# Performance work log

Measured on AMD Instinct MI355X. Metric: run time of the kernel, lower is better.

## Reference

```python
import jax, jax.numpy as jnp
import numpy as np

B, L, T = 64, 256, 800
NMEL, PRE, ARNN, DRNN, ENC, ATT, NF, K = 80, 256, 512, 512, 512, 128, 32, 31
ZP = 0.1  # zoneout prob (eval-mode expected-value interpolation)


def setup_inputs() -> dict:
    key = jax.random.key(0)
    ks = iter(jax.random.split(key, 32))
    def p(shape, s=0.05):
        return jax.random.normal(next(ks), shape, dtype=jnp.float32) * s
    inp = {
        'encoder_out': jax.random.normal(next(ks), (B, L, ENC), dtype=jnp.float32),
        'lengths': jax.random.randint(next(ks), (B,), L // 2, L + 1),
        'mels': jax.random.normal(next(ks), (B, T, NMEL), dtype=jnp.float32),
        # prenet: 3 bias-free linears with relu (eval: dropout off)
        'Wp1': p((PRE, NMEL)), 'Wp2': p((PRE, PRE)), 'Wp3': p((PRE, PRE)),
        # attention LSTMCell: input = prenet_dim + enc = 768
        'aWih': p((4 * ARNN, PRE + ENC)), 'aWhh': p((4 * ARNN, ARNN)),
        'abih': jnp.zeros((4 * ARNN,)), 'abhh': jnp.zeros((4 * ARNN,)),
        # decoder LSTMCell: input = att_rnn + enc = 1024
        'dWih': p((4 * DRNN, ARNN + ENC)), 'dWhh': p((4 * DRNN, DRNN)),
        'dbih': jnp.zeros((4 * DRNN,)), 'dbhh': jnp.zeros((4 * DRNN,)),
        # location-sensitive attention (all bias-free)
        'Wq': p((ATT, ARNN)), 'Wm': p((ATT, ENC)),
        'Wconv': p((NF, 2, K)), 'Wloc': p((ATT, NF)), 'v': p((1, ATT)),
        # output projection + gate
        'Wout': p((NMEL, DRNN + ENC)), 'bout': jnp.zeros((NMEL,)),
        'Wgate': p((1, DRNN + ENC)), 'bgate': jnp.zeros((1,)),
    }
    return inp


def _lstm(x, h, c, Wih, Whh, bih, bhh):
    g = x @ Wih.T + h @ Whh.T + (bih + bhh)
    i, f, gg, o = jnp.split(g, 4, axis=-1)
    c2 = jax.nn.sigmoid(f) * c + jax.nn.sigmoid(i) * jnp.tanh(gg)
    return jax.nn.sigmoid(o) * jnp.tanh(c2), c2


def _zoneout(new, old):
    return ZP * old + (1.0 - ZP) * new


def decoder_forward(encoder_out, lengths, mels, Wp1, Wp2, Wp3,
                    aWih, aWhh, abih, abhh, dWih, dWhh, dbih, dbhh,
                    Wq, Wm, Wconv, Wloc, v, Wout, bout, Wgate, bgate):
    b, l, _ = encoder_out.shape
    t = mels.shape[1]
    processed_memory = encoder_out @ Wm.T                       # (B,L,ATT)
    mask = jnp.arange(l)[None, :] >= lengths[:, None]           # True = padded
    # teacher forcing inputs: shift mels right by one zero frame
    dec_in = jnp.concatenate(
        [jnp.zeros((b, 1, NMEL), encoder_out.dtype), mels[:, :t - 1]], axis=1)
    xs = jnp.swapaxes(dec_in, 0, 1)                             # (T,B,NMEL)

    def step(carry, frame):
        ah, ac, dh, dc, ctx, aw, aws = carry
        x = jax.nn.relu(jax.nn.relu(jax.nn.relu(frame @ Wp1.T) @ Wp2.T) @ Wp3.T)
        ah2, ac2 = _lstm(jnp.concatenate([x, ctx], -1), ah, ac, aWih, aWhh, abih, abhh)
        ah2, ac2 = _zoneout(ah2, ah), _zoneout(ac2, ac)
        # location features: conv over (B,2,L)
        aw_cat = jnp.stack([aw, aws], axis=1)
        loc = jax.lax.conv_general_dilated(
            aw_cat, Wconv, window_strides=(1,), padding=[((K - 1) // 2,) * 2],
            dimension_numbers=('NCH', 'OIH', 'NCH'))                # (B,NF,L)
        ploc = jnp.swapaxes(loc, 1, 2) @ Wloc.T                      # (B,L,ATT)
        e = jnp.tanh(ah2[:, None, :] @ Wq.T + processed_memory + ploc)
        energies = jnp.squeeze(e @ v.T, -1)                          # (B,L)
        energies = jnp.where(mask, jnp.float32(-1e9), energies)
        w = jax.nn.softmax(energies, axis=-1)
        ctx2 = jnp.einsum('bl,ble->be', w, encoder_out)
        aws2 = aws + w
        dh2, dc2 = _lstm(jnp.concatenate([ah2, ctx2], -1), dh, dc, dWih, dWhh, dbih, dbhh)
        dh2, dc2 = _zoneout(dh2, dh), _zoneout(dc2, dc)
        dhc = jnp.concatenate([dh2, ctx2], axis=-1)
        mel = dhc @ Wout.T + bout
        gate = jnp.squeeze(dhc @ Wgate.T + bgate, -1)
        return (ah2, ac2, dh2, dc2, ctx2, w, aws2), (mel, gate, w)

    z = lambda *s: jnp.zeros(s, encoder_out.dtype)
    carry0 = (z(b, ARNN), z(b, ARNN), z(b, DRNN), z(b, DRNN), z(b, ENC), z(b, l), z(b, l))
    _, (mel_t, gate_t, align_t) = jax.lax.scan(step, carry0, xs)
    return (jnp.swapaxes(mel_t, 0, 1),      # (B,T,NMEL)
            jnp.swapaxes(gate_t, 0, 1),     # (B,T)
            jnp.swapaxes(align_t, 0, 1))    # (B,T,L)


def reference(encoder_out, lengths, mels, Wp1, Wp2, Wp3,
              aWih, aWhh, abih, abhh, dWih, dWhh, dbih, dbhh,
              Wq, Wm, Wconv, Wloc, v, Wout, bout, Wgate, bgate):
    return decoder_forward(encoder_out, lengths, mels, Wp1, Wp2, Wp3,
                           aWih, aWhh, abih, abhh, dWih, dWhh, dbih, dbhh,
                           Wq, Wm, Wconv, Wloc, v, Wout, bout, Wgate, bgate)
```

## Files before the change

kernel.cpp:

```cpp
#include <hip/hip_runtime.h>


#define DEV_INLINE __device__ __forceinline__

constexpr int TB = 800;

constexpr size_t PMT_O  = 0;
constexpr size_t WQT_O  = 2228224;
constexpr size_t LOCF_O = 2293760;
constexpr size_t Y1_O   = 2818048;
constexpr size_t Y2_O   = 2834432;
constexpr size_t XR_O   = 2850816;
constexpr size_t AH_O   = 2883584;
constexpr size_t AC_O   = 2949120;
constexpr size_t DH_O   = 3014656;
constexpr size_t DC_O   = 3080192;
constexpr size_t CTX_O  = 3145728;
constexpr size_t AW_O   = 3211264;
constexpr size_t AWS_O  = 3244032;
constexpr size_t BAR_O  = 3276800;
constexpr size_t ZERO_N = 991232;

constexpr size_t MEL_O  = 0;
constexpr size_t GATE_O = 4096000;
constexpr size_t ALG_O  = 4147200;

DEV_INLINE float sigf(float x)     { return 1.0f / (1.0f + __expf(-x)); }
DEV_INLINE float tanhfast(float x) { float e = __expf(2.0f * x); return 1.0f - 2.0f / (e + 1.0f); }

DEV_INLINE void stc(float* p, float v) {
  __hip_atomic_store(p, v, __ATOMIC_RELAXED, __HIP_MEMORY_SCOPE_AGENT);
}

struct Params {
  const float* enc; const int* len; const float* mels;
  const float* Wp1; const float* Wp2; const float* Wp3;
  const float* aWih; const float* aWhh; const float* abih; const float* abhh;
  const float* dWih; const float* dWhh; const float* dbih; const float* dbhh;
  const float* Wconv; const float* Wloc; const float* v;
  const float* Wout; const float* bout; const float* Wgate; const float* bgate;
  float* ws; float* out;
};

DEV_INLINE void gbar(unsigned* bar, int blk, bool iscap, unsigned e)
{
  __syncthreads();
  if (threadIdx.x == 0) {
    const unsigned g = (unsigned)blk >> 5;
    unsigned a = __hip_atomic_fetch_add(bar + g * 64, 1u, __ATOMIC_RELAXED, __HIP_MEMORY_SCOPE_AGENT);
    if (a == e * 32u - 1u)
      __hip_atomic_fetch_add(bar + 512, 1u, __ATOMIC_RELAXED, __HIP_MEMORY_SCOPE_AGENT);
    if (iscap) {
      while (__hip_atomic_load(bar + 512, __ATOMIC_RELAXED, __HIP_MEMORY_SCOPE_AGENT) < e * 8u)
        __builtin_amdgcn_s_sleep(1);
      __builtin_amdgcn_fence(__ATOMIC_ACQUIRE, "agent");
      const unsigned nc = __hip_atomic_load(bar + 2176, __ATOMIC_RELAXED, __HIP_MEMORY_SCOPE_AGENT);
      unsigned c = __hip_atomic_fetch_add(bar + 576, 1u, __ATOMIC_RELAXED, __HIP_MEMORY_SCOPE_AGENT);
      if (c == e * nc - 1u) {
#pragma unroll
        for (unsigned i = 0; i < 8; ++i)
          __hip_atomic_store(bar + 640 + i * 64, e, __ATOMIC_RELAXED, __HIP_MEMORY_SCOPE_AGENT);
      }
    }
    {
      const unsigned g2 = (unsigned)blk >> 5;
      while (__hip_atomic_load(bar + 640 + g2 * 64, __ATOMIC_RELAXED, __HIP_MEMORY_SCOPE_AGENT) < e)
        __builtin_amdgcn_s_sleep(4);
    }
  }
  __syncthreads();
  asm volatile("buffer_inv sc0\n\ts_waitcnt vmcnt(0)" ::: "memory");
}

DEV_INLINE void gseg16(float* __restrict__ acc,
                       const float* __restrict__ inT,
                       const float* __restrict__ W, const int ldw, const int wcol0,
                       const int u0, const int segk0, const int seglen,
                       const int ks, const int ke, const int lane)
{
  const int a0 = ks > segk0 ? ks : segk0;
  const int a1 = (ke < segk0 + seglen) ? ke : (segk0 + seglen);
  if (a0 >= a1) return;
  const float* __restrict__ ip = inT + (size_t)(a0 - segk0) * 64 + lane;
  const int n = a1 - a0;
  const float* wp[16];
#pragma unroll
  for (int j = 0; j < 16; ++j) {
    const int row = u0 + (j >> 2) + 512 * (j & 3);
    wp[j] = W + (size_t)row * ldw + (wcol0 + (a0 - segk0));
  }
  for (int k = 0; k < n; k += 4) {
    const float x0 = ip[(k + 0) * 64];
    const float x1 = ip[(k + 1) * 64];
    const float x2 = ip[(k + 2) * 64];
    const float x3 = ip[(k + 3) * 64];
#pragma unroll
    for (int j = 0; j < 16; ++j)
      acc[j] += x0 * wp[j][k] + x1 * wp[j][k + 1] + x2 * wp[j][k + 2] + x3 * wp[j][k + 3];
  }
}

template<int NO>
DEV_INLINE void gseg(float* __restrict__ acc,
                     const float* __restrict__ inT,
                     const float* __restrict__ W, const int ldw, const int wcol0,
                     const int* __restrict__ rows, const int segk0, const int seglen,
                     const int ks, const int ke, const int lane)
{
  const int a0 = ks > segk0 ? ks : segk0;
  const int a1 = (ke < segk0 + seglen) ? ke : (segk0 + seglen);
  if (a0 >= a1) return;
  const float* __restrict__ ip = inT + (size_t)(a0 - segk0) * 64 + lane;
  const int n = a1 - a0;
  const float* wp[NO];
#pragma unroll
  for (int j = 0; j < NO; ++j)
    wp[j] = W + (size_t)rows[j] * ldw + (wcol0 + (a0 - segk0));
  for (int k = 0; k < n; k += 4) {
    const float x0 = ip[(k + 0) * 64];
    const float x1 = ip[(k + 1) * 64];
    const float x2 = ip[(k + 2) * 64];
    const float x3 = ip[(k + 3) * 64];
#pragma unroll
    for (int j = 0; j < NO; ++j)
      acc[j] += x0 * wp[j][k] + x1 * wp[j][k + 1] + x2 * wp[j][k + 2] + x3 * wp[j][k + 3];
  }
}

__global__ __launch_bounds__(256) void init_kernel(const float* __restrict__ Wq,
                                                   float* __restrict__ ws)
{
  const int i = blockIdx.x * 256 + threadIdx.x;
  {
    const int k = i >> 7, a = i & 127;
    ws[WQT_O + i] = Wq[a * 512 + k];
  }
  for (size_t idx = i; idx < ZERO_N; idx += 65536)
    ws[LOCF_O + idx] = 0.0f;
}

__global__ __launch_bounds__(256) void prenet_kernel(const float* __restrict__ mels,
                                                     const float* __restrict__ Wp1,
                                                     const float* __restrict__ Wp2,
                                                     const float* __restrict__ Wp3,
                                                     float* __restrict__ xb)
{
  __shared__ float smem[16384];
  const int t = blockIdx.x;
  const int tid = threadIdx.x;
  const int lane = tid & 63;
  const int wv = __builtin_amdgcn_readfirstlane(tid >> 6);

  if (t == 0) {
    for (int i = tid; i < 5200; i += 256) smem[i] = 0.0f;
  } else {
    for (int i = tid; i < 5120; i += 256) {
      const int b = i / 80, k = i - b * 80;
      smem[k * 65 + b] = mels[((size_t)b * TB + (t - 1)) * 80 + k];
    }
  }
  __syncthreads();

  float va[8][8];
#pragma unroll
  for (int g = 0; g < 8; ++g) {
    const int u0 = wv * 64 + g * 8;
    float acc[8] = {};
    for (int k = 0; k < 80; ++k) {
      const float x = smem[k * 65 + lane];
#pragma unroll
      for (int j = 0; j < 8; ++j) acc[j] += x * Wp1[(u0 + j) * 80 + k];
    }
#pragma unroll
    for (int j = 0; j < 8; ++j) va[g][j] = fmaxf(acc[j], 0.0f);
  }
  __syncthreads();
#pragma unroll
  for (int g = 0; g < 8; ++g)
#pragma unroll
    for (int j = 0; j < 8; ++j) smem[(wv * 64 + g * 8 + j) * 64 + lane] = va[g][j];
  __syncthreads();

#pragma unroll
  for (int g = 0; g < 8; ++g) {
    const int u0 = wv * 64 + g * 8;
    float acc[8] = {};
    for (int k = 0; k < 256; ++k) {
      const float x = smem[k * 64 + lane];
#pragma unroll
      for (int j = 0; j < 8; ++j) acc[j] += x * Wp2[(u0 + j) * 256 + k];
    }
#pragma unroll
    for (int j = 0; j < 8; ++j) va[g][j] = fmaxf(acc[j], 0.0f);
  }
  __syncthreads();
#pragma unroll
  for (int g = 0; g < 8; ++g)
#pragma unroll
    for (int j = 0; j < 8; ++j) smem[(wv * 64 + g * 8 + j) * 64 + lane] = va[g][j];
  __syncthreads();

#pragma unroll
  for (int g = 0; g < 8; ++g) {
    const int u0 = wv * 64 + g * 8;
    float acc[8] = {};
    for (int k = 0; k < 256; ++k) {
      const float x = smem[k * 64 + lane];
#pragma unroll
      for (int j = 0; j < 8; ++j) acc[j] += x * Wp3[(u0 + j) * 256 + k];
    }
#pragma unroll
    for (int j = 0; j < 8; ++j)
      xb[((size_t)t * 256 + (u0 + j)) * 64 + lane] = fmaxf(acc[j], 0.0f);
  }
}

__global__ __launch_bounds__(256) void pm_kernel(const float* __restrict__ enc,
                                                 const float* __restrict__ Wm,
                                                 float* __restrict__ pmT)
{
  __shared__ float encL[64 * 129];
  const int b = blockIdx.x >> 2;
  const int l0 = (blockIdx.x & 3) * 64;
  const int tid = threadIdx.x;
  const int lane = tid & 63;
  const int wv = __builtin_amdgcn_readfirstlane(tid >> 6);

  float acc[4][8];
#pragma unroll
  for (int ai = 0; ai < 4; ++ai)
#pragma unroll
    for (int j = 0; j < 8; ++j) acc[ai][j] = 0.0f;

  for (int kc = 0; kc < 4; ++kc) {
    __syncthreads();
    for (int i = tid; i < 64 * 128; i += 256) {
      const int l = i >> 7, k = i & 127;
      encL[l * 129 + k] = enc[((size_t)b * 256 + l0 + l) * 512 + kc * 128 + k];
    }
    __syncthreads();
#pragma unroll
    for (int ai = 0; ai < 4; ++ai) {
      const int agrp = (ai * 4 + wv) * 8;
      for (int k = 0; k < 128; ++k) {
        const float x = encL[lane * 129 + k];
#pragma unroll
        for (int j = 0; j < 8; ++j)
          acc[ai][j] += x * Wm[(size_t)(agrp + j) * 512 + kc * 128 + k];
      }
    }
  }
#pragma unroll
  for (int ai = 0; ai < 4; ++ai) {
    const int agrp = (ai * 4 + wv) * 8;
#pragma unroll
    for (int j = 0; j < 8; ++j)
      pmT[((size_t)b * 128 + agrp + j) * 256 + l0 + lane] = acc[ai][j];
  }
}


DEV_INLINE void f_dgates4(int u0, int tid, int lane, int wv,
                          const float* __restrict__ ah, const float* __restrict__ dh,
                          float* __restrict__ gdL, const Params& p, float* sm)
{
  float acc[16] = {};
  const int ks = wv * 256, ke = ks + 256;
  gseg16(acc, ah, p.dWih, 1024, 0, u0, 0,   512, ks, ke, lane);
  gseg16(acc, dh, p.dWhh, 512,  0, u0, 512, 512, ks, ke, lane);
#pragma unroll
  for (int j = 0; j < 16; ++j) sm[(wv * 16 + j) * 64 + lane] = acc[j];
  __syncthreads();
  {
    const int m = tid & 63, uq = tid >> 6;
    const int u = u0 + uq;
#pragma unroll
    for (int q = 0; q < 4; ++q) {
      const int j = uq * 4 + q;
      gdL[j * 64 + m] = sm[j * 64 + m] + sm[(16 + j) * 64 + m] + sm[(32 + j) * 64 + m] + sm[(48 + j) * 64 + m]
                      + p.dbih[u + 512 * q] + p.dbhh[u + 512 * q];
    }
  }
  __syncthreads();
}

DEV_INLINE void f_dfin4(int u0, int tid, int lane, int wv,
                        const float* __restrict__ ctx, const float* __restrict__ gdL,
                        float* __restrict__ dh_o, float* __restrict__ dhL, float* __restrict__ dcL,
                        const Params& p, float* sm)
{
  float acc[16] = {};
  const int ks = wv * 128, ke = ks + 128;
  gseg16(acc, ctx, p.dWih, 1024, 512, u0, 0, 512, ks, ke, lane);
#pragma unroll
  for (int j = 0; j < 16; ++j) sm[(wv * 16 + j) * 64 + lane] = acc[j];
  __syncthreads();
  {
    const int m = tid & 63, uq = tid >> 6;
    const int u = u0 + uq;
    float g[4];
#pragma unroll
    for (int q = 0; q < 4; ++q) {
      const int j = uq * 4 + q;
      g[q] = sm[j * 64 + m] + sm[(16 + j) * 64 + m] + sm[(32 + j) * 64 + m] + sm[(48 + j) * 64 + m]
           + gdL[j * 64 + m];
    }
    const float ho = dhL[uq * 64 + m], co = dcL[uq * 64 + m];
    const float c2 = sigf(g[1]) * co + sigf(g[0]) * tanhfast(g[2]);
    const float h2 = sigf(g[3]) * tanhfast(c2);
    const float hn = 0.1f * ho + 0.9f * h2;
    const float cn = 0.1f * co + 0.9f * c2;
    stc(dh_o + (size_t)u * 64 + m, hn);
    dhL[uq * 64 + m] = hn;
    dcL[uq * 64 + m] = cn;
  }
  __syncthreads();
}

DEV_INLINE void f_alstm4(int u0, int tid, int lane, int wv,
                         const float* __restrict__ xt, const float* __restrict__ ctx,
                         const float* __restrict__ ahg,
                         float* __restrict__ ah_o, float* __restrict__ ahL, float* __restrict__ acL,
                         const Params& p, float* sm)
{
  float acc[16] = {};
  const int ks = wv * 320, ke = ks + 320;
  gseg16(acc, xt,  p.aWih, 768, 0,   u0, 0,   256, ks, ke, lane);
  gseg16(acc, ctx, p.aWih, 768, 256, u0, 256, 512, ks, ke, lane);
  gseg16(acc, ahg, p.aWhh, 512, 0,   u0, 768, 512, ks, ke, lane);
#pragma unroll
  for (int j = 0; j < 16; ++j) sm[(wv * 16 + j) * 64 + lane] = acc[j];
  __syncthreads();
  {
    const int m = tid & 63, uq = tid >> 6;
    const int u = u0 + uq;
    float g[4];
#pragma unroll
    for (int q = 0; q < 4; ++q) {
      const int j = uq * 4 + q;
      g[q] = sm[j * 64 + m] + sm[(16 + j) * 64 + m] + sm[(32 + j) * 64 + m] + sm[(48 + j) * 64 + m]
           + p.abih[u + 512 * q] + p.abhh[u + 512 * q];
    }
    const float ho = ahL[uq * 64 + m], co = acL[uq * 64 + m];
    const float c2 = sigf(g[1]) * co + sigf(g[0]) * tanhfast(g[2]);
    const float h2 = sigf(g[3]) * tanhfast(c2);
    const float hn = 0.1f * ho + 0.9f * h2;
    const float cn = 0.1f * co + 0.9f * c2;
    stc(ah_o + (size_t)u * 64 + m, hn);
    ahL[uq * 64 + m] = hn;
    acL[uq * 64 + m] = cn;
  }
  __syncthreads();
}

DEV_INLINE void f_mel(int c0, int tid, int lane, int wv, int tm1,
                      const float* __restrict__ dh, const float* __restrict__ ctx,
                      const Params& p, float* sm)
{
  int rows[4] = {c0, c0 + 1, c0 + 2, c0 + 3};
  float acc[4] = {};
  const int ks = wv * 256, ke = ks + 256;
  gseg<4>(acc, dh,  p.Wout, 1024, 0,   rows, 0,   512, ks, ke, lane);
  gseg<4>(acc, ctx, p.Wout, 1024, 512, rows, 512, 512, ks, ke, lane);
#pragma unroll
  for (int j = 0; j < 4; ++j) sm[(wv * 4 + j) * 64 + lane] = acc[j];
  __syncthreads();
  {
    const int m = tid & 63, c = tid >> 6;
    const float val = sm[c * 64 + m] + sm[(4 + c) * 64 + m] + sm[(8 + c) * 64 + m] + sm[(12 + c) * 64 + m]
                    + p.bout[c0 + c];
    stc(p.out + MEL_O + ((size_t)m * TB + tm1) * 80 + c0 + c, val);
  }
  __syncthreads();
}

DEV_INLINE void f_gate(int tid, int lane, int wv, int tm1,
                       const float* __restrict__ dh, const float* __restrict__ ctx,
                       const Params& p, float* sm)
{
  float acc[1] = {};
  int rows1[1] = {0};
  const int ks = wv * 256, ke = ks + 256;
  gseg<1>(acc, dh,  p.Wgate, 1024, 0,   rows1, 0,   512, ks, ke, lane);
  gseg<1>(acc, ctx, p.Wgate, 1024, 512, rows1, 512, 512, ks, ke, lane);
  sm[wv * 64 + lane] = acc[0];
  __syncthreads();
  if (tid < 64) {
    const float val = sm[tid] + sm[64 + tid] + sm[128 + tid] + sm[192 + tid] + p.bgate[0];
    stc(p.out + GATE_O + (size_t)tid * TB + tm1, val);
  }
  __syncthreads();
}

DEV_INLINE void f_conv(int b, int tid,
                       const float* __restrict__ aw, const float* __restrict__ aws,
                       float* __restrict__ locF, const Params& p, float* sm)
{
  float* awL  = sm;
  float* awsL = sm + 290;
  if (tid < 15) { awL[tid] = 0.0f; awsL[tid] = 0.0f; awL[271 + tid] = 0.0f; awsL[271 + tid] = 0.0f; }
  awL[15 + tid]  = aw[b * 256 + tid];
  awsL[15 + tid] = aws[b * 256 + tid];
  __syncthreads();
  float awv[31], awsv[31];
#pragma unroll
  for (int k = 0; k < 31; ++k) { awv[k] = awL[tid + k]; awsv[k] = awsL[tid + k]; }
  float* dst = locF + ((size_t)b * 256 + tid) * 32;
  for (int f = 0; f < 32; ++f) {
    const float* wc = p.Wconv + f * 62;
    float lf = 0.0f;
#pragma unroll
    for (int k = 0; k < 31; ++k) lf += awv[k] * wc[k] + awsv[k] * wc[31 + k];
    stc(dst + f, lf);
  }
  __syncthreads();
}

DEV_INLINE void f_energy(int b, int t, int tid, int lane, int wv,
                         const float* __restrict__ ah, const float* __restrict__ aws_p,
                         float* __restrict__ ctx_o, float* __restrict__ aw_o,
                         float* __restrict__ aws_o,
                         const float* __restrict__ pmT, const float* __restrict__ wqT,
                         const float* __restrict__ locF, const Params& p, float* sm)
{
  float* ahL = sm;
  float* qpL = sm + 512;
  float* qL  = sm + 768;
  float* red = sm + 896;
  float* wL  = sm + 912;
  ahL[tid]       = ah[(size_t)tid * 64 + b];
  ahL[tid + 256] = ah[(size_t)(tid + 256) * 64 + b];
  __syncthreads();
  {
    const int a = tid & 127, h = tid >> 7;
    float qp = 0.0f;
    const float* wq = wqT + (size_t)(h * 256) * 128 + a;
    const float* xv = ahL + h * 256;
    for (int k = 0; k < 256; k += 4)
      qp += wq[(k + 0) * 128] * xv[k + 0] + wq[(k + 1) * 128] * xv[k + 1]
          + wq[(k + 2) * 128] * xv[k + 2] + wq[(k + 3) * 128] * xv[k + 3];
    qpL[tid] = qp;
  }
  __syncthreads();
  if (tid < 128) qL[tid] = qpL[tid] + qpL[128 + tid];
  __syncthreads();

  float locv[32];
  {
    const float4* lf4 = (const float4*)(locF + ((size_t)b * 256 + tid) * 32);
#pragma unroll
    for (int i = 0; i < 8; ++i) {
      float4 x = lf4[i];
      locv[4*i] = x.x; locv[4*i+1] = x.y; locv[4*i+2] = x.z; locv[4*i+3] = x.w;
    }
  }
  float part = 0.0f;
  const float* pmp = pmT + (size_t)b * 32768 + tid;
#pragma unroll 2
  for (int a = 0; a < 128; ++a) {
    float s = qL[a] + pmp[(size_t)a * 256];
    const float* wl = p.Wloc + a * 32;
#pragma unroll
    for (int f = 0; f < 32; ++f) s += locv[f] * wl[f];
    part += p.v[a] * tanhfast(s);
  }
  if (tid >= p.len[b]) part = -1e9f;

  float mv = part;
  for (int mm = 32; mm >= 1; mm >>= 1) mv = fmaxf(mv, __shfl_xor(mv, mm, 64));
  if (lane == 0) red[wv] = mv;
  __syncthreads();
  const float mx = fmaxf(fmaxf(red[0], red[1]), fmaxf(red[2], red[3]));
  const float pex = __expf(part - mx);
  float ssum = pex;
  for (int mm = 32; mm >= 1; mm >>= 1) ssum += __shfl_xor(ssum, mm, 64);
  if (lane == 0) red[8 + wv] = ssum;
  __syncthreads();
  const float inv = 1.0f / (red[8] + red[9] + red[10] + red[11]);
  const float w = pex * inv;
  wL[tid] = w;
  stc(aw_o + b * 256 + tid, w);
  stc(aws_o + b * 256 + tid, aws_p[b * 256 + tid] + w);
  stc(p.out + ALG_O + ((size_t)b * TB + t) * 256 + tid, w);
  __syncthreads();

  float c0 = 0.0f, c1 = 0.0f;
  const float* ep = p.enc + (size_t)b * 256 * 512;
  for (int l = 0; l < 256; ++l) {
    const float wv_ = wL[l];
    c0 += wv_ * ep[(size_t)l * 512 + tid];
    c1 += wv_ * ep[(size_t)l * 512 + tid + 256];
  }
  stc(ctx_o + (size_t)tid * 64 + b, c0);
  stc(ctx_o + (size_t)(tid + 256) * 64 + b, c1);
  __syncthreads();
}

DEV_INLINE void f_pn1(int blkL, int frame, int lane, int wv,
                      const Params& p, float* __restrict__ y1)
{
  const int u0 = blkL * 32 + wv * 8;
  float acc[8] = {};
  const float* mp = p.mels + ((size_t)lane * TB + frame) * 80;
  for (int k = 0; k < 80; ++k) {
    const float x = mp[k];
#pragma unroll
    for (int j = 0; j < 8; ++j) acc[j] += x * p.Wp1[(u0 + j) * 80 + k];
  }
#pragma unroll
  for (int j = 0; j < 8; ++j) stc(y1 + (size_t)(u0 + j) * 64 + lane, fmaxf(acc[j], 0.0f));
}

DEV_INLINE void f_pnmid(int blkL, int lane, int wv,
                        const float* __restrict__ yin, const float* __restrict__ W,
                        float* __restrict__ yout)
{
  const int u0 = blkL * 32 + wv * 8;
  float acc[8] = {};
  for (int k = 0; k < 256; ++k) {
    const float x = yin[(size_t)k * 64 + lane];
#pragma unroll
    for (int j = 0; j < 8; ++j) acc[j] += x * W[(u0 + j) * 256 + k];
  }
#pragma unroll
  for (int j = 0; j < 8; ++j) stc(yout + (size_t)(u0 + j) * 64 + lane, fmaxf(acc[j], 0.0f));
}

__global__ __launch_bounds__(256) void persist_kernel(Params p)
{
  __shared__ float sm[4096];
  __shared__ float gdL[1024];
  __shared__ float s1L[256];
  __shared__ float s2L[256];
  __shared__ unsigned capflag;

  const int tid = threadIdx.x, blk = blockIdx.x;
  const int lane = tid & 63;
  const int wv = __builtin_amdgcn_readfirstlane(tid >> 6);
  const bool isX = blk < 128;
  const int yi = blk - 128;

  float* ws   = p.ws;
  float* pmT  = ws + PMT_O;
  float* wqT  = ws + WQT_O;
  float* locF = ws + LOCF_O;
  float* y1   = ws + Y1_O;
  float* y2   = ws + Y2_O;
  float* xr   = ws + XR_O;
  float* AH[2]  = {ws + AH_O,  ws + AH_O  + 32768};
  float* DH[2]  = {ws + DH_O,  ws + DH_O  + 32768};
  float* CTX[2] = {ws + CTX_O, ws + CTX_O + 32768};
  float* AW[2]  = {ws + AW_O,  ws + AW_O  + 16384};
  float* AWS[2] = {ws + AWS_O, ws + AWS_O + 16384};
  unsigned* bar = (unsigned*)(ws + BAR_O);

  s1L[tid] = 0.0f; s2L[tid] = 0.0f;
  if (tid == 0) {
    unsigned x;
    asm volatile("s_getreg_b32 %0, hwreg(HW_REG_XCC_ID)" : "=s"(x));
    unsigned prev = __hip_atomic_fetch_add(bar + 2048 + (x & 7), 1u,
                                           __ATOMIC_RELAXED, __HIP_MEMORY_SCOPE_AGENT);
    if (prev == 0)
      __hip_atomic_fetch_add(bar + 2176, 1u, __ATOMIC_RELAXED, __HIP_MEMORY_SCOPE_AGENT);
    capflag = (prev == 0) ? 1u : 0u;
  }
  __syncthreads();
  const bool iscap = (capflag != 0);
  unsigned e = 0;

  if (!isX && yi >= 85 && yi < 93) f_pn1(yi - 85, 1, lane, wv, p, y1);
  gbar(bar, blk, iscap, ++e);

  if (!isX) {
    f_alstm4(yi * 4, tid, lane, wv, xr, CTX[1], AH[1], AH[0], s1L, s2L, p, sm);
  } else if (blk < 8) {
    f_pnmid(blk, lane, wv, y1, p.Wp2, y2);
  }
  gbar(bar, blk, iscap, ++e);

  for (int t = 0; t < TB; ++t) {
    const int cur = t & 1, prv = cur ^ 1;
    if (isX) {
      f_dgates4(blk * 4, tid, lane, wv, AH[cur], DH[prv], gdL, p, sm);
    } else if (yi < 64) {
      f_energy(yi, t, tid, lane, wv, AH[cur], AWS[prv],
               CTX[cur], AW[cur], AWS[cur], pmT, wqT, locF, p, sm);
    } else if (yi < 84) {
      if (t > 0) f_mel((yi - 64) * 4, tid, lane, wv, t - 1, DH[prv], CTX[prv], p, sm);
    } else if (yi == 84) {
      if (t > 0) f_gate(tid, lane, wv, t - 1, DH[prv], CTX[prv], p, sm);
    } else if (yi < 93) {
      if (t <= 796) f_pn1(yi - 85, t + 2, lane, wv, p, y1);
    } else if (yi < 101) {
      if (t <= 797) f_pnmid(yi - 93, lane, wv, y2, p.Wp3, xr + (size_t)cur * 16384);
    }
    gbar(bar, blk, iscap, ++e);

    if (isX) {
      f_dfin4(blk * 4, tid, lane, wv, CTX[cur], gdL, DH[cur], s1L, s2L, p, sm);
      if (blk >= 64) {
        if (t < TB - 1) f_conv(blk - 64, tid, AW[cur], AWS[cur], locF, p, sm);
      } else if (blk < 8) {
        if (t <= 796) f_pnmid(blk, lane, wv, y1, p.Wp2, y2);
      }
    } else {
      if (t < TB - 1)
        f_alstm4(yi * 4, tid, lane, wv, xr + (size_t)prv * 16384, CTX[cur],
                 AH[cur], AH[prv], s1L, s2L, p, sm);
    }
    gbar(bar, blk, iscap, ++e);
  }
  if (!isX) {
    if (yi >= 64 && yi < 84)  f_mel((yi - 64) * 4, tid, lane, wv, TB - 1, DH[1], CTX[1], p, sm);
    else if (yi == 84)        f_gate(tid, lane, wv, TB - 1, DH[1], CTX[1], p, sm);
  }
}

extern "C" void kernel_launch(void* const* d_in, const int* in_sizes, int n_in,
                              void* d_out, int out_size, void* d_ws, size_t ws_size,
                              hipStream_t stream)
{
  (void)in_sizes; (void)n_in; (void)out_size; (void)ws_size;
  Params P;
  P.enc   = (const float*)d_in[0];
  P.len   = (const int*)  d_in[1];
  P.mels  = (const float*)d_in[2];
  P.Wp1   = (const float*)d_in[3];
  P.Wp2   = (const float*)d_in[4];
  P.Wp3   = (const float*)d_in[5];
  P.aWih  = (const float*)d_in[6];
  P.aWhh  = (const float*)d_in[7];
  P.abih  = (const float*)d_in[8];
  P.abhh  = (const float*)d_in[9];
  P.dWih  = (const float*)d_in[10];
  P.dWhh  = (const float*)d_in[11];
  P.dbih  = (const float*)d_in[12];
  P.dbhh  = (const float*)d_in[13];
  const float* Wq = (const float*)d_in[14];
  const float* Wm = (const float*)d_in[15];
  P.Wconv = (const float*)d_in[16];
  P.Wloc  = (const float*)d_in[17];
  P.v     = (const float*)d_in[18];
  P.Wout  = (const float*)d_in[19];
  P.bout  = (const float*)d_in[20];
  P.Wgate = (const float*)d_in[21];
  P.bgate = (const float*)d_in[22];
  P.ws  = (float*)d_ws;
  P.out = (float*)d_out;

  init_kernel<<<256, 256, 0, stream>>>(Wq, P.ws);
  pm_kernel<<<256, 256, 0, stream>>>(P.enc, Wm, P.ws + PMT_O);
  prenet_kernel<<<2, 256, 0, stream>>>(P.mels, P.Wp1, P.Wp2, P.Wp3, P.ws + XR_O);

  persist_kernel<<<256, 256, 0, stream>>>(P);
}
```

Baseline: 101.8 ms.

## Cache per-block LSTM gate weights and Wloc in LDS for persistent kernel

At kernel start, each persistent block copies its 16 rows of decoder or attention LSTM weights into dynamic shared memory. They are stored transposed and interleaved so that one k index yields four float4 loads covering all 16 outputs. Attention-energy blocks also stage Wloc in shared memory. The per-timestep GEMV loops then read weights from LDS, where all lanes hit the same address, instead of re-fetching them from global memory/L2 on each of the 800 steps. The cost is about 120KB of dynamic LDS per block plus a one-time staging load.

Result: slower. 224.9 ms (+120.9%).

```diff
diff --git a/kernel.cpp b/kernel.cpp
--- a/kernel.cpp
+++ b/kernel.cpp
@@ -12,9 +12,7 @@
 constexpr size_t Y2_O   = 2834432;
 constexpr size_t XR_O   = 2850816;
 constexpr size_t AH_O   = 2883584;
-constexpr size_t AC_O   = 2949120;
 constexpr size_t DH_O   = 3014656;
-constexpr size_t DC_O   = 3080192;
 constexpr size_t CTX_O  = 3145728;
 constexpr size_t AW_O   = 3211264;
 constexpr size_t AWS_O  = 3244032;
@@ -24,6 +22,16 @@
 constexpr size_t MEL_O  = 0;
 constexpr size_t GATE_O = 4096000;
 constexpr size_t ALG_O  = 4147200;
+
+constexpr int L_WDG = 0;
+constexpr int L_WDF = 16384;
+constexpr int L_WAL = 0;
+constexpr int L_WLOC= 20480;
+constexpr int L_SM  = 24576;
+constexpr int L_GD  = 28672;
+constexpr int L_S1  = 29696;
+constexpr int L_S2  = 29952;
+constexpr int L_TOT = 30208;
 
 DEV_INLINE float sigf(float x)     { return 1.0f / (1.0f + __expf(-x)); }
 DEV_INLINE float tanhfast(float x) { float e = __expf(2.0f * x); return 1.0f - 2.0f / (e + 1.0f); }
@@ -72,31 +80,33 @@
   asm volatile("buffer_inv sc0\n\ts_waitcnt vmcnt(0)" ::: "memory");
 }
 
-DEV_INLINE void gseg16(float* __restrict__ acc,
-                       const float* __restrict__ inT,
-                       const float* __restrict__ W, const int ldw, const int wcol0,
-                       const int u0, const int segk0, const int seglen,
-                       const int ks, const int ke, const int lane)
+DEV_INLINE void gseg16L(float* __restrict__ acc,
+                        const float* __restrict__ inT,
+                        const float4* __restrict__ w4,
+                        const int segk0, const int seglen,
+                        const int ks, const int ke, const int lane)
 {
   const int a0 = ks > segk0 ? ks : segk0;
   const int a1 = (ke < segk0 + seglen) ? ke : (segk0 + seglen);
   if (a0 >= a1) return;
   const float* __restrict__ ip = inT + (size_t)(a0 - segk0) * 64 + lane;
+  const float4* __restrict__ wp = w4 + (size_t)a0 * 4;
   const int n = a1 - a0;
-  const float* wp[16];
-#pragma unroll
-  for (int j = 0; j < 16; ++j) {
-    const int row = u0 + (j >> 2) + 512 * (j & 3);
-    wp[j] = W + (size_t)row * ldw + (wcol0 + (a0 - segk0));
-  }
-  for (int k = 0; k < n; k += 4) {
+  for (int k = 0; k < n; k += 2) {
     const float x0 = ip[(k + 0) * 64];
     const float x1 = ip[(k + 1) * 64];
-    const float x2 = ip[(k + 2) * 64];
-    const float x3 = ip[(k + 3) * 64];
-#pragma unroll
-    for (int j = 0; j < 16; ++j)
-      acc[j] += x0 * wp[j][k] + x1 * wp[j][k + 1] + x2 * wp[j][k + 2] + x3 * wp[j][k + 3];
+#pragma unroll
+    for (int h = 0; h < 2; ++h) {
+      const float x = h ? x1 : x0;
+      const float4 w0 = wp[(k + h) * 4 + 0];
+      const float4 w1 = wp[(k + h) * 4 + 1];
+      const float4 w2 = wp[(k + h) * 4 + 2];
+      const float4 w3 = wp[(k + h) * 4 + 3];
+      acc[0]  += x * w0.x;  acc[1]  += x * w0.y;  acc[2]  += x * w0.z;  acc[3]  += x * w0.w;
+      acc[4]  += x * w1.x;  acc[5]  += x * w1.y;  acc[6]  += x * w1.z;  acc[7]  += x * w1.w;
+      acc[8]  += x * w2.x;  acc[9]  += x * w2.y;  acc[10] += x * w2.z;  acc[11] += x * w2.w;
+      acc[12] += x * w3.x;  acc[13] += x * w3.y;  acc[14] += x * w3.z;  acc[15] += x * w3.w;
+    }
   }
 }
 
@@ -262,12 +272,13 @@
 
 DEV_INLINE void f_dgates4(int u0, int tid, int lane, int wv,
                           const float* __restrict__ ah, const float* __restrict__ dh,
-                          float* __restrict__ gdL, const Params& p, float* sm)
+                          float* __restrict__ gdL, const float4* __restrict__ wDG4,
+                          const Params& p, float* sm)
 {
   float acc[16] = {};
   const int ks = wv * 256, ke = ks + 256;
-  gseg16(acc, ah, p.dWih, 1024, 0, u0, 0,   512, ks, ke, lane);
-  gseg16(acc, dh, p.dWhh, 512,  0, u0, 512, 512, ks, ke, lane);
+  gseg16L(acc, ah, wDG4, 0,   512, ks, ke, lane);
+  gseg16L(acc, dh, wDG4, 512, 512, ks, ke, lane);
 #pragma unroll
   for (int j = 0; j < 16; ++j) sm[(wv * 16 + j) * 64 + lane] = acc[j];
   __syncthreads();
@@ -287,11 +298,11 @@
 DEV_INLINE void f_dfin4(int u0, int tid, int lane, int wv,
                         const float* __restrict__ ctx, const float* __restrict__ gdL,
                         float* __restrict__ dh_o, float* __restrict__ dhL, float* __restrict__ dcL,
-                        const Params& p, float* sm)
+                        const float4* __restrict__ wDF4, const Params& p, float* sm)
 {
   float acc[16] = {};
   const int ks = wv * 128, ke = ks + 128;
-  gseg16(acc, ctx, p.dWih, 1024, 512, u0, 0, 512, ks, ke, lane);
+  gseg16L(acc, ctx, wDF4, 0, 512, ks, ke, lane);
 #pragma unroll
   for (int j = 0; j < 16; ++j) sm[(wv * 16 + j) * 64 + lane] = acc[j];
   __syncthreads();
@@ -321,13 +332,13 @@
                          const float* __restrict__ xt, const float* __restrict__ ctx,
                          const float* __restrict__ ahg,
                          float* __restrict__ ah_o, float* __restrict__ ahL, float* __restrict__ acL,
-                         const Params& p, float* sm)
+                         const float4* __restrict__ wAL4, const Params& p, float* sm)
 {
   float acc[16] = {};
   const int ks = wv * 320, ke = ks + 320;
-  gseg16(acc, xt,  p.aWih, 768, 0,   u0, 0,   256, ks, ke, lane);
-  gseg16(acc, ctx, p.aWih, 768, 256, u0, 256, 512, ks, ke, lane);
-  gseg16(acc, ahg, p.aWhh, 512, 0,   u0, 768, 512, ks, ke, lane);
+  gseg16L(acc, xt,  wAL4, 0,   256, ks, ke, lane);
+  gseg16L(acc, ctx, wAL4, 256, 512, ks, ke, lane);
+  gseg16L(acc, ahg, wAL4, 768, 512, ks, ke, lane);
 #pragma unroll
   for (int j = 0; j < 16; ++j) sm[(wv * 16 + j) * 64 + lane] = acc[j];
   __syncthreads();
@@ -421,7 +432,8 @@
                          float* __restrict__ ctx_o, float* __restrict__ aw_o,
                          float* __restrict__ aws_o,
                          const float* __restrict__ pmT, const float* __restrict__ wqT,
-                         const float* __restrict__ locF, const Params& p, float* sm)
+                         const float* __restrict__ locF, const float* __restrict__ wlocL,
+                         const Params& p, float* sm)
 {
   float* ahL = sm;
   float* qpL = sm + 512;
@@ -459,7 +471,7 @@
 #pragma unroll 2
   for (int a = 0; a < 128; ++a) {
     float s = qL[a] + pmp[(size_t)a * 256];
-    const float* wl = p.Wloc + a * 32;
+    const float* wl = wlocL + a * 32;
 #pragma unroll
     for (int f = 0; f < 32; ++f) s += locv[f] * wl[f];
     part += p.v[a] * tanhfast(s);
@@ -528,10 +540,7 @@
 
 __global__ __launch_bounds__(256) void persist_kernel(Params p)
 {
-  __shared__ float sm[4096];
-  __shared__ float gdL[1024];
-  __shared__ float s1L[256];
-  __shared__ float s2L[256];
+  extern __shared__ float lds[];
   __shared__ unsigned capflag;
 
   const int tid = threadIdx.x, blk = blockIdx.x;
@@ -539,6 +548,15 @@
   const int wv = __builtin_amdgcn_readfirstlane(tid >> 6);
   const bool isX = blk < 128;
   const int yi = blk - 128;
+
+  float* sm  = lds + L_SM;
+  float* gdL = lds + L_GD;
+  float* s1L = lds + L_S1;
+  float* s2L = lds + L_S2;
+  const float4* wDG4 = (const float4*)(lds + L_WDG);
+  const float4* wDF4 = (const float4*)(lds + L_WDF);
+  const float4* wAL4 = (const float4*)(lds + L_WAL);
+  float* wlocL = lds + L_WLOC;
 
   float* ws   = p.ws;
   float* pmT  = ws + PMT_O;
@@ -554,6 +572,36 @@
   float* AWS[2] = {ws + AWS_O, ws + AWS_O + 16384};
   unsigned* bar = (unsigned*)(ws + BAR_O);
 
+  if (isX) {
+    const int u0 = blk * 4;
+    float* wDG = lds + L_WDG;
+    float* wDF = lds + L_WDF;
+#pragma unroll
+    for (int j = 0; j < 16; ++j) {
+      const int row = u0 + (j >> 2) + 512 * (j & 3);
+      const float* dwih = p.dWih + (size_t)row * 1024;
+      const float* dwhh = p.dWhh + (size_t)row * 512;
+      for (int k = tid; k < 512; k += 256) {
+        wDG[k * 16 + j]         = dwih[k];
+        wDG[(512 + k) * 16 + j] = dwhh[k];
+        wDF[k * 16 + j]         = dwih[512 + k];
+      }
+    }
+  } else {
+    const int u0 = yi * 4;
+    float* wAL = lds + L_WAL;
+#pragma unroll
+    for (int j = 0; j < 16; ++j) {
+      const int row = u0 + (j >> 2) + 512 * (j & 3);
+      const float* awih = p.aWih + (size_t)row * 768;
+      const float* awhh = p.aWhh + (size_t)row * 512;
+      for (int k = tid; k < 768; k += 256) wAL[k * 16 + j] = awih[k];
+      for (int k = tid; k < 512; k += 256) wAL[(768 + k) * 16 + j] = awhh[k];
+    }
+    if (yi < 64)
+      for (int i = tid; i < 4096; i += 256) wlocL[i] = p.Wloc[i];
+  }
+
   s1L[tid] = 0.0f; s2L[tid] = 0.0f;
   if (tid == 0) {
     unsigned x;
@@ -572,7 +620,7 @@
   gbar(bar, blk, iscap, ++e);
 
   if (!isX) {
-    f_alstm4(yi * 4, tid, lane, wv, xr, CTX[1], AH[1], AH[0], s1L, s2L, p, sm);
+    f_alstm4(yi * 4, tid, lane, wv, xr, CTX[1], AH[1], AH[0], s1L, s2L, wAL4, p, sm);
   } else if (blk < 8) {
     f_pnmid(blk, lane, wv, y1, p.Wp2, y2);
   }
@@ -581,10 +629,10 @@
   for (int t = 0; t < TB; ++t) {
     const int cur = t & 1, prv = cur ^ 1;
     if (isX) {
-      f_dgates4(blk * 4, tid, lane, wv, AH[cur], DH[prv], gdL, p, sm);
+      f_dgates4(blk * 4, tid, lane, wv, AH[cur], DH[prv], gdL, wDG4, p, sm);
     } else if (yi < 64) {
       f_energy(yi, t, tid, lane, wv, AH[cur], AWS[prv],
-               CTX[cur], AW[cur], AWS[cur], pmT, wqT, locF, p, sm);
+               CTX[cur], AW[cur], AWS[cur], pmT, wqT, locF, wlocL, p, sm);
     } else if (yi < 84) {
       if (t > 0) f_mel((yi - 64) * 4, tid, lane, wv, t - 1, DH[prv], CTX[prv], p, sm);
     } else if (yi == 84) {
@@ -597,7 +645,7 @@
     gbar(bar, blk, iscap, ++e);
 
     if (isX) {
-      f_dfin4(blk * 4, tid, lane, wv, CTX[cur], gdL, DH[cur], s1L, s2L, p, sm);
+      f_dfin4(blk * 4, tid, lane, wv, CTX[cur], gdL, DH[cur], s1L, s2L, wDF4, p, sm);
       if (blk >= 64) {
         if (t < TB - 1) f_conv(blk - 64, tid, AW[cur], AWS[cur], locF, p, sm);
       } else if (blk < 8) {
@@ -606,7 +654,7 @@
     } else {
       if (t < TB - 1)
         f_alstm4(yi * 4, tid, lane, wv, xr + (size_t)prv * 16384, CTX[cur],
-                 AH[cur], AH[prv], s1L, s2L, p, sm);
+                 AH[cur], AH[prv], s1L, s2L, wAL4, p, sm);
     }
     gbar(bar, blk, iscap, ++e);
   }
@@ -648,9 +696,15 @@
   P.ws  = (float*)d_ws;
   P.out = (float*)d_out;
 
+  const int dsz = L_TOT * 4;
+  static int attr_done = 0;
+  (void)attr_done;
+  hipFuncSetAttribute((const void*)persist_kernel,
+                      hipFuncAttributeMaxDynamicSharedMemorySize, dsz);
+
   init_kernel<<<256, 256, 0, stream>>>(Wq, P.ws);
   pm_kernel<<<256, 256, 0, stream>>>(P.enc, Wm, P.ws + PMT_O);
   prenet_kernel<<<2, 256, 0, stream>>>(P.mels, P.Wp1, P.Wp2, P.Wp3, P.ws + XR_O);
 
-  persist_kernel<<<256, 256, 0, stream>>>(P);
-}
+  persist_kernel<<<256, 256, dsz, stream>>>(P);
+}
```

## Double persistent blocks to two per CU, halving LSTM units per block

Applied to the files above, without the earlier changes.

The persistent kernel now launches 512 blocks with launch bounds for two resident blocks per CU. Each LSTM block handles 2 hidden units instead of 4, and X and Y roles are interleaved by block parity. The grid barrier groups are widened to 64 blocks. Energy blocks also cache Wloc in shared memory, and the context loop is unrolled. The goal is more wavefronts to hide memory latency in the serial recurrent step, at the cost of more barrier participants, reduced shared memory per block and a hard requirement that two blocks fit on each CU.

Result: slower. 205.3 ms (+101.6%).

```diff
diff --git a/kernel.cpp b/kernel.cpp
--- a/kernel.cpp
+++ b/kernel.cpp
@@ -4,6 +4,7 @@
 #define DEV_INLINE __device__ __forceinline__
 
 constexpr int TB = 800;
+constexpr unsigned NBLK = 512;
 
 constexpr size_t PMT_O  = 0;
 constexpr size_t WQT_O  = 2228224;
@@ -12,9 +13,7 @@
 constexpr size_t Y2_O   = 2834432;
 constexpr size_t XR_O   = 2850816;
 constexpr size_t AH_O   = 2883584;
-constexpr size_t AC_O   = 2949120;
 constexpr size_t DH_O   = 3014656;
-constexpr size_t DC_O   = 3080192;
 constexpr size_t CTX_O  = 3145728;
 constexpr size_t AW_O   = 3211264;
 constexpr size_t AWS_O  = 3244032;
@@ -46,9 +45,9 @@
 {
   __syncthreads();
   if (threadIdx.x == 0) {
-    const unsigned g = (unsigned)blk >> 5;
+    const unsigned g = (unsigned)blk >> 6;
     unsigned a = __hip_atomic_fetch_add(bar + g * 64, 1u, __ATOMIC_RELAXED, __HIP_MEMORY_SCOPE_AGENT);
-    if (a == e * 32u - 1u)
+    if (a == e * 64u - 1u)
       __hip_atomic_fetch_add(bar + 512, 1u, __ATOMIC_RELAXED, __HIP_MEMORY_SCOPE_AGENT);
     if (iscap) {
       while (__hip_atomic_load(bar + 512, __ATOMIC_RELAXED, __HIP_MEMORY_SCOPE_AGENT) < e * 8u)
@@ -63,7 +62,7 @@
       }
     }
     {
-      const unsigned g2 = (unsigned)blk >> 5;
+      const unsigned g2 = (unsigned)blk >> 6;
       while (__hip_atomic_load(bar + 640 + g2 * 64, __ATOMIC_RELAXED, __HIP_MEMORY_SCOPE_AGENT) < e)
         __builtin_amdgcn_s_sleep(4);
     }
@@ -72,20 +71,20 @@
   asm volatile("buffer_inv sc0\n\ts_waitcnt vmcnt(0)" ::: "memory");
 }
 
-DEV_INLINE void gseg16(float* __restrict__ acc,
-                       const float* __restrict__ inT,
-                       const float* __restrict__ W, const int ldw, const int wcol0,
-                       const int u0, const int segk0, const int seglen,
-                       const int ks, const int ke, const int lane)
+DEV_INLINE void gseg8(float* __restrict__ acc,
+                      const float* __restrict__ inT,
+                      const float* __restrict__ W, const int ldw, const int wcol0,
+                      const int u0, const int segk0, const int seglen,
+                      const int ks, const int ke, const int lane)
 {
   const int a0 = ks > segk0 ? ks : segk0;
   const int a1 = (ke < segk0 + seglen) ? ke : (segk0 + seglen);
   if (a0 >= a1) return;
   const float* __restrict__ ip = inT + (size_t)(a0 - segk0) * 64 + lane;
   const int n = a1 - a0;
-  const float* wp[16];
-#pragma unroll
-  for (int j = 0; j < 16; ++j) {
+  const float* wp[8];
+#pragma unroll
+  for (int j = 0; j < 8; ++j) {
     const int row = u0 + (j >> 2) + 512 * (j & 3);
     wp[j] = W + (size_t)row * ldw + (wcol0 + (a0 - segk0));
   }
@@ -95,7 +94,7 @@
     const float x2 = ip[(k + 2) * 64];
     const float x3 = ip[(k + 3) * 64];
 #pragma unroll
-    for (int j = 0; j < 16; ++j)
+    for (int j = 0; j < 8; ++j)
       acc[j] += x0 * wp[j][k] + x1 * wp[j][k + 1] + x2 * wp[j][k + 2] + x3 * wp[j][k + 3];
   }
 }
@@ -260,49 +259,49 @@
 }
 
 
-DEV_INLINE void f_dgates4(int u0, int tid, int lane, int wv,
+DEV_INLINE void f_dgates2(int u0, int tid, int lane, int wv,
                           const float* __restrict__ ah, const float* __restrict__ dh,
                           float* __restrict__ gdL, const Params& p, float* sm)
 {
-  float acc[16] = {};
+  float acc[8] = {};
   const int ks = wv * 256, ke = ks + 256;
-  gseg16(acc, ah, p.dWih, 1024, 0, u0, 0,   512, ks, ke, lane);
-  gseg16(acc, dh, p.dWhh, 512,  0, u0, 512, 512, ks, ke, lane);
-#pragma unroll
-  for (int j = 0; j < 16; ++j) sm[(wv * 16 + j) * 64 + lane] = acc[j];
-  __syncthreads();
-  {
+  gseg8(acc, ah, p.dWih, 1024, 0, u0, 0,   512, ks, ke, lane);
+  gseg8(acc, dh, p.dWhh, 512,  0, u0, 512, 512, ks, ke, lane);
+#pragma unroll
+  for (int j = 0; j < 8; ++j) sm[(wv * 8 + j) * 64 + lane] = acc[j];
+  __syncthreads();
+  if (tid < 128) {
     const int m = tid & 63, uq = tid >> 6;
     const int u = u0 + uq;
 #pragma unroll
     for (int q = 0; q < 4; ++q) {
       const int j = uq * 4 + q;
-      gdL[j * 64 + m] = sm[j * 64 + m] + sm[(16 + j) * 64 + m] + sm[(32 + j) * 64 + m] + sm[(48 + j) * 64 + m]
+      gdL[j * 64 + m] = sm[j * 64 + m] + sm[(8 + j) * 64 + m] + sm[(16 + j) * 64 + m] + sm[(24 + j) * 64 + m]
                       + p.dbih[u + 512 * q] + p.dbhh[u + 512 * q];
     }
   }
   __syncthreads();
 }
 
-DEV_INLINE void f_dfin4(int u0, int tid, int lane, int wv,
+DEV_INLINE void f_dfin2(int u0, int tid, int lane, int wv,
                         const float* __restrict__ ctx, const float* __restrict__ gdL,
                         float* __restrict__ dh_o, float* __restrict__ dhL, float* __restrict__ dcL,
                         const Params& p, float* sm)
 {
-  float acc[16] = {};
+  float acc[8] = {};
   const int ks = wv * 128, ke = ks + 128;
-  gseg16(acc, ctx, p.dWih, 1024, 512, u0, 0, 512, ks, ke, lane);
-#pragma unroll
-  for (int j = 0; j < 16; ++j) sm[(wv * 16 + j) * 64 + lane] = acc[j];
-  __syncthreads();
-  {
+  gseg8(acc, ctx, p.dWih, 1024, 512, u0, 0, 512, ks, ke, lane);
+#pragma unroll
+  for (int j = 0; j < 8; ++j) sm[(wv * 8 + j) * 64 + lane] = acc[j];
+  __syncthreads();
+  if (tid < 128) {
     const int m = tid & 63, uq = tid >> 6;
     const int u = u0 + uq;
     float g[4];
 #pragma unroll
     for (int q = 0; q < 4; ++q) {
       const int j = uq * 4 + q;
-      g[q] = sm[j * 64 + m] + sm[(16 + j) * 64 + m] + sm[(32 + j) * 64 + m] + sm[(48 + j) * 64 + m]
+      g[q] = sm[j * 64 + m] + sm[(8 + j) * 64 + m] + sm[(16 + j) * 64 + m] + sm[(24 + j) * 64 + m]
            + gdL[j * 64 + m];
     }
     const float ho = dhL[uq * 64 + m], co = dcL[uq * 64 + m];
@@ -317,28 +316,28 @@
   __syncthreads();
 }
 
-DEV_INLINE void f_alstm4(int u0, int tid, int lane, int wv,
+DEV_INLINE void f_alstm2(int u0, int tid, int lane, int wv,
                          const float* __restrict__ xt, const float* __restrict__ ctx,
                          const float* __restrict__ ahg,
                          float* __restrict__ ah_o, float* __restrict__ ahL, float* __restrict__ acL,
                          const Params& p, float* sm)
 {
-  float acc[16] = {};
+  float acc[8] = {};
   const int ks = wv * 320, ke = ks + 320;
-  gseg16(acc, xt,  p.aWih, 768, 0,   u0, 0,   256, ks, ke, lane);
-  gseg16(acc, ctx, p.aWih, 768, 256, u0, 256, 512, ks, ke, lane);
-  gseg16(acc, ahg, p.aWhh, 512, 0,   u0, 768, 512, ks, ke, lane);
-#pragma unroll
-  for (int j = 0; j < 16; ++j) sm[(wv * 16 + j) * 64 + lane] = acc[j];
-  __syncthreads();
-  {
+  gseg8(acc, xt,  p.aWih, 768, 0,   u0, 0,   256, ks, ke, lane);
+  gseg8(acc, ctx, p.aWih, 768, 256, u0, 256, 512, ks, ke, lane);
+  gseg8(acc, ahg, p.aWhh, 512, 0,   u0, 768, 512, ks, ke, lane);
+#pragma unroll
+  for (int j = 0; j < 8; ++j) sm[(wv * 8 + j) * 64 + lane] = acc[j];
+  __syncthreads();
+  if (tid < 128) {
     const int m = tid & 63, uq = tid >> 6;
     const int u = u0 + uq;
     float g[4];
 #pragma unroll
     for (int q = 0; q < 4; ++q) {
       const int j = uq * 4 + q;
-      g[q] = sm[j * 64 + m] + sm[(16 + j) * 64 + m] + sm[(32 + j) * 64 + m] + sm[(48 + j) * 64 + m]
+      g[q] = sm[j * 64 + m] + sm[(8 + j) * 64 + m] + sm[(16 + j) * 64 + m] + sm[(24 + j) * 64 + m]
            + p.abih[u + 512 * q] + p.abhh[u + 512 * q];
     }
     const float ho = ahL[uq * 64 + m], co = acL[uq * 64 + m];
@@ -421,7 +420,8 @@
                          float* __restrict__ ctx_o, float* __restrict__ aw_o,
                          float* __restrict__ aws_o,
                          const float* __restrict__ pmT, const float* __restrict__ wqT,
-                         const float* __restrict__ locF, const Params& p, float* sm)
+                         const float* __restrict__ locF, const float* __restrict__ wlocL,
+                         const Params& p, float* sm)
 {
   float* ahL = sm;
   float* qpL = sm + 512;
@@ -459,7 +459,7 @@
 #pragma unroll 2
   for (int a = 0; a < 128; ++a) {
     float s = qL[a] + pmp[(size_t)a * 256];
-    const float* wl = p.Wloc + a * 32;
+    const float* wl = wlocL + a * 32;
 #pragma unroll
     for (int f = 0; f < 32; ++f) s += locv[f] * wl[f];
     part += p.v[a] * tanhfast(s);
@@ -486,6 +486,7 @@
 
   float c0 = 0.0f, c1 = 0.0f;
   const float* ep = p.enc + (size_t)b * 256 * 512;
+#pragma unroll 4
   for (int l = 0; l < 256; ++l) {
     const float wv_ = wL[l];
     c0 += wv_ * ep[(size_t)l * 512 + tid];
@@ -526,19 +527,21 @@
   for (int j = 0; j < 8; ++j) stc(yout + (size_t)(u0 + j) * 64 + lane, fmaxf(acc[j], 0.0f));
 }
 
-__global__ __launch_bounds__(256) void persist_kernel(Params p)
-{
-  __shared__ float sm[4096];
-  __shared__ float gdL[1024];
-  __shared__ float s1L[256];
-  __shared__ float s2L[256];
+__global__ __launch_bounds__(256, 2) void persist_kernel(Params p)
+{
+  __shared__ float sm[2048];
+  __shared__ float gdL[512];
+  __shared__ float s1L[128];
+  __shared__ float s2L[128];
+  __shared__ float wlocL[4096];
   __shared__ unsigned capflag;
 
   const int tid = threadIdx.x, blk = blockIdx.x;
   const int lane = tid & 63;
   const int wv = __builtin_amdgcn_readfirstlane(tid >> 6);
-  const bool isX = blk < 128;
-  const int yi = blk - 128;
+  const bool isX = (blk & 1) == 0;
+  const int bx = blk >> 1;
+  const int by = blk >> 1;
 
   float* ws   = p.ws;
   float* pmT  = ws + PMT_O;
@@ -554,7 +557,10 @@
   float* AWS[2] = {ws + AWS_O, ws + AWS_O + 16384};
   unsigned* bar = (unsigned*)(ws + BAR_O);
 
-  s1L[tid] = 0.0f; s2L[tid] = 0.0f;
+  if (!isX && by < 64)
+    for (int i = tid; i < 4096; i += 256) wlocL[i] = p.Wloc[i];
+
+  if (tid < 128) { s1L[tid] = 0.0f; s2L[tid] = 0.0f; }
   if (tid == 0) {
     unsigned x;
     asm volatile("s_getreg_b32 %0, hwreg(HW_REG_XCC_ID)" : "=s"(x));
@@ -568,51 +574,51 @@
   const bool iscap = (capflag != 0);
   unsigned e = 0;
 
-  if (!isX && yi >= 85 && yi < 93) f_pn1(yi - 85, 1, lane, wv, p, y1);
+  if (!isX && by >= 85 && by < 93) f_pn1(by - 85, 1, lane, wv, p, y1);
   gbar(bar, blk, iscap, ++e);
 
   if (!isX) {
-    f_alstm4(yi * 4, tid, lane, wv, xr, CTX[1], AH[1], AH[0], s1L, s2L, p, sm);
-  } else if (blk < 8) {
-    f_pnmid(blk, lane, wv, y1, p.Wp2, y2);
+    f_alstm2(by * 2, tid, lane, wv, xr, CTX[1], AH[1], AH[0], s1L, s2L, p, sm);
+  } else if (bx < 8) {
+    f_pnmid(bx, lane, wv, y1, p.Wp2, y2);
   }
   gbar(bar, blk, iscap, ++e);
 
   for (int t = 0; t < TB; ++t) {
     const int cur = t & 1, prv = cur ^ 1;
     if (isX) {
-      f_dgates4(blk * 4, tid, lane, wv, AH[cur], DH[prv], gdL, p, sm);
-    } else if (yi < 64) {
-      f_energy(yi, t, tid, lane, wv, AH[cur], AWS[prv],
-               CTX[cur], AW[cur], AWS[cur], pmT, wqT, locF, p, sm);
-    } else if (yi < 84) {
-      if (t > 0) f_mel((yi - 64) * 4, tid, lane, wv, t - 1, DH[prv], CTX[prv], p, sm);
-    } else if (yi == 84) {
+      f_dgates2(bx * 2, tid, lane, wv, AH[cur], DH[prv], gdL, p, sm);
+    } else if (by < 64) {
+      f_energy(by, t, tid, lane, wv, AH[cur], AWS[prv],
+               CTX[cur], AW[cur], AWS[cur], pmT, wqT, locF, wlocL, p, sm);
+    } else if (by < 84) {
+      if (t > 0) f_mel((by - 64) * 4, tid, lane, wv, t - 1, DH[prv], CTX[prv], p, sm);
+    } else if (by == 84) {
       if (t > 0) f_gate(tid, lane, wv, t - 1, DH[prv], CTX[prv], p, sm);
-    } else if (yi < 93) {
-      if (t <= 796) f_pn1(yi - 85, t + 2, lane, wv, p, y1);
-    } else if (yi < 101) {
-      if (t <= 797) f_pnmid(yi - 93, lane, wv, y2, p.Wp3, xr + (size_t)cur * 16384);
+    } else if (by < 93) {
+      if (t <= 796) f_pn1(by - 85, t + 2, lane, wv, p, y1);
+    } else if (by < 101) {
+      if (t <= 797) f_pnmid(by - 93, lane, wv, y2, p.Wp3, xr + (size_t)cur * 16384);
     }
     gbar(bar, blk, iscap, ++e);
 
     if (isX) {
-      f_dfin4(blk * 4, tid, lane, wv, CTX[cur], gdL, DH[cur], s1L, s2L, p, sm);
-      if (blk >= 64) {
-        if (t < TB - 1) f_conv(blk - 64, tid, AW[cur], AWS[cur], locF, p, sm);
-      } else if (blk < 8) {
-        if (t <= 796) f_pnmid(blk, lane, wv, y1, p.Wp2, y2);
+      f_dfin2(bx * 2, tid, lane, wv, CTX[cur], gdL, DH[cur], s1L, s2L, p, sm);
+      if (bx >= 192) {
+        if (t < TB - 1) f_conv(bx - 192, tid, AW[cur], AWS[cur], locF, p, sm);
+      } else if (bx < 8) {
+        if (t <= 796) f_pnmid(bx, lane, wv, y1, p.Wp2, y2);
       }
     } else {
       if (t < TB - 1)
-        f_alstm4(yi * 4, tid, lane, wv, xr + (size_t)prv * 16384, CTX[cur],
+        f_alstm2(by * 2, tid, lane, wv, xr + (size_t)prv * 16384, CTX[cur],
                  AH[cur], AH[prv], s1L, s2L, p, sm);
     }
     gbar(bar, blk, iscap, ++e);
   }
   if (!isX) {
-    if (yi >= 64 && yi < 84)  f_mel((yi - 64) * 4, tid, lane, wv, TB - 1, DH[1], CTX[1], p, sm);
-    else if (yi == 84)        f_gate(tid, lane, wv, TB - 1, DH[1], CTX[1], p, sm);
+    if (by >= 64 && by < 84)  f_mel((by - 64) * 4, tid, lane, wv, TB - 1, DH[1], CTX[1], p, sm);
+    else if (by == 84)        f_gate(tid, lane, wv, TB - 1, DH[1], CTX[1], p, sm);
   }
 }
 
@@ -652,5 +658,5 @@
   pm_kernel<<<256, 256, 0, stream>>>(P.enc, Wm, P.ws + PMT_O);
   prenet_kernel<<<2, 256, 0, stream>>>(P.mels, P.Wp1, P.Wp2, P.Wp3, P.ws + XR_O);
 
-  persist_kernel<<<256, 256, 0, stream>>>(P);
-}
+  persist_kernel<<<NBLK, 256, 0, stream>>>(P);
+}
```
